# Kernel tuning notes

Hardware: AMD Instinct MI355X
Metric: run time of the kernel (lower is better)

The kernel has to match this reference:

```python
import jax, jax.numpy as jnp
import numpy as np

S, P, C, H, K = 16, 512, 768, 12, 6
D = C // H


def setup_inputs() -> dict:
    key = jax.random.key(0)
    k0, k1, k2 = jax.random.split(key, 3)
    x = jax.random.normal(k0, (1, S * P, C), jnp.float32)
    Wqkv = jax.random.normal(k1, (C, 3 * C), jnp.float32) * (C ** -0.5)
    bqkv = jnp.zeros((3 * C,), jnp.float32)
    Wproj = jax.random.normal(k2, (C, C), jnp.float32) * (C ** -0.5)
    bproj = jnp.zeros((C,), jnp.float32)
    # each frame i is covisible with K frames (itself + K-1 temporal neighbours)
    covis_idx = jnp.asarray((np.arange(S)[:, None] + np.arange(K)[None, :]) % S,
                            jnp.int32)  # [S, K]
    return {"x": x, "Wqkv": Wqkv, "bqkv": bqkv,
            "Wproj": Wproj, "bproj": bproj, "covis_idx": covis_idx}


def reference(x, Wqkv, bqkv, Wproj, bproj, covis_idx):
    B, N, C_ = x.shape
    S_, K_ = covis_idx.shape
    P_ = N // S_
    # qkv projection -> [3, B, H, N, D]
    qkv = (x @ Wqkv + bqkv).reshape(B, N, 3, H, D).transpose(2, 0, 3, 1, 4)
    q, k, v = qkv[0], qkv[1], qkv[2]
    kf = k.reshape(B, H, S_, P_, D)          # keys grouped by frame
    vf = v.reshape(B, H, S_, P_, D)
    qf = q.reshape(B, H, S_, P_, D).transpose(2, 0, 1, 3, 4)  # [S,B,H,P,D]
    scale = jnp.float32(D) ** -0.5

    def step(_, inp):
        q_i, idx = inp                        # q_i [B,H,P,D], idx [K]
        k_c = kf[:, :, idx].reshape(B, H, K_ * P_, D)   # gather covisible tokens
        v_c = vf[:, :, idx].reshape(B, H, K_ * P_, D)
        s = jnp.einsum('bhpd,bhnd->bhpn', q_i, k_c) * scale
        a = jax.nn.softmax(s, axis=-1)
        return None, jnp.einsum('bhpn,bhnd->bhpd', a, v_c)

    _, out = jax.lax.scan(step, None, (qf, covis_idx))  # [S,B,H,P,D]
    out = out.transpose(1, 0, 3, 2, 4).reshape(B, N, C_)  # [B, S*P, H*D]
    return out @ Wproj + bproj
```

## Files before the change

kernel.cpp:

```cpp
#include <hip/hip_runtime.h>
#include <stdint.h>

typedef __bf16 bf16;
typedef __bf16 bf16x4 __attribute__((ext_vector_type(4)));
typedef __bf16 bf16x8 __attribute__((ext_vector_type(8)));
typedef float floatx4 __attribute__((ext_vector_type(4)));
typedef short short4v __attribute__((ext_vector_type(4)));

#define NTOK 8192
#define HEADSZ 524288L

#if defined(__has_builtin)
#if __has_builtin(__builtin_amdgcn_mfma_f32_16x16x16bf16_1k)
#define HAVE_MFMA16_BUILTIN 1
#endif
#endif
__device__ __forceinline__ floatx4 mfma16(short4v a, short4v b, floatx4 c) {
#ifdef HAVE_MFMA16_BUILTIN
  return __builtin_amdgcn_mfma_f32_16x16x16bf16_1k(a, b, c, 0, 0, 0);
#else
  floatx4 d;
  asm("v_mfma_f32_16x16x16_bf16 %0, %1, %2, %3" : "=v"(d) : "v"(a), "v"(b), "v"(c));
  return d;
#endif
}

__device__ __forceinline__ void gload16(const bf16* g, bf16* l) {
  __builtin_amdgcn_global_load_lds(
      (const __attribute__((address_space(1))) uint8_t*)g,
      (__attribute__((address_space(3))) uint8_t*)l, 16, 0, 0);
}

__global__ void detect_kernel(const unsigned short* __restrict__ x, int* __restrict__ flag) {
  int lane = threadIdx.x & 63;
  int cnt = 0;
#pragma unroll
  for (int i = 0; i < 4; ++i) {
    unsigned int u = x[2 * (lane * 4 + i)];
    float v = __uint_as_float(u << 16);
    if (!(fabsf(v) <= 1e4f)) cnt++;
  }
#pragma unroll
  for (int off = 1; off < 64; off <<= 1) cnt += __shfl_xor(cnt, off, 64);
  if (threadIdx.x == 0) *flag = (cnt > 32) ? 1 : 0;
}

__global__ __launch_bounds__(256) void ingest_kernel(
    const void* s0, const void* s1, const void* s2, const void* s3, const void* s4,
    bf16* d0, bf16* d1, bf16* d2, bf16* d3, bf16* d4,
    const int* __restrict__ flag) {
  const long b0 = 6291456, b1 = b0 + 1769472, b2 = b1 + 2304, b3 = b2 + 589824, b4 = b3 + 768;
  long g = ((long)blockIdx.x * 256 + threadIdx.x) * 8;
  if (g >= b4) return;
  const void* src; bf16* dst; long off;
  if (g < b0)      { src = s0; dst = d0; off = g; }
  else if (g < b1) { src = s1; dst = d1; off = g - b0; }
  else if (g < b2) { src = s2; dst = d2; off = g - b1; }
  else if (g < b3) { src = s3; dst = d3; off = g - b2; }
  else             { src = s4; dst = d4; off = g - b3; }
  if (*flag) {
    const float* s = (const float*)src + off;
#pragma unroll
    for (int e = 0; e < 8; ++e) dst[off + e] = (bf16)s[e];
  } else {
    *(uint4*)(dst + off) = *(const uint4*)((const bf16*)src + off);
  }
}

__global__ __launch_bounds__(256) void transpose_kernel(
    const bf16* __restrict__ in, bf16* __restrict__ out, int R, int Ccols) {
  __shared__ bf16 t[32][33];
  int bx = blockIdx.x * 32, by = blockIdx.y * 32;
  int tx = threadIdx.x & 31, ty = threadIdx.x >> 5;
#pragma unroll
  for (int i = ty; i < 32; i += 8) t[i][tx] = in[(long)(by + i) * Ccols + bx + tx];
  __syncthreads();
#pragma unroll
  for (int i = ty; i < 32; i += 8) out[(long)(bx + i) * R + by + tx] = t[tx][i];
}

template <int EPI>
__global__ __launch_bounds__(256, 2) void gemm_kernel(
    const bf16* __restrict__ A, const bf16* __restrict__ BT,
    const bf16* __restrict__ bias, void* __restrict__ Cout,
    int M, int N, int Kd, const int* __restrict__ flag) {
  __shared__ bf16 As[128 * 32];
  __shared__ bf16 Bs[128 * 32];
  const int tid = threadIdx.x;
  const int w = tid >> 6, lane = tid & 63;
  const int quad = lane >> 4, l15 = lane & 15;
  const int m0 = blockIdx.x * 128, n0 = blockIdx.y * 128;
  const int wm = w >> 1, wn = w & 1;
  const int srow = lane >> 2;
  const int scol = (lane & 3) * 8;

  floatx4 acc[4][4] = {};
  const bf16* ga = A + (long)(m0 + 32 * w + srow) * Kd + scol;
  const bf16* gb = BT + (long)(n0 + 32 * w + srow) * Kd + scol;
  bf16* la = As + 32 * w * 32;
  bf16* lb = Bs + 32 * w * 32;

  for (int kk = 0; kk < Kd; kk += 32) {
    __syncthreads();
    gload16(ga + kk, la);
    gload16(ga + kk + 16 * Kd, la + 16 * 32);
    gload16(gb + kk, lb);
    gload16(gb + kk + 16 * Kd, lb + 16 * 32);
    __syncthreads();
    bf16x8 fa[4], fb[4];
#pragma unroll
    for (int i = 0; i < 4; ++i)
      fa[i] = *(const bf16x8*)(As + (64 * wm + 16 * i + l15) * 32 + quad * 8);
#pragma unroll
    for (int j = 0; j < 4; ++j)
      fb[j] = *(const bf16x8*)(Bs + (64 * wn + 16 * j + l15) * 32 + quad * 8);
#pragma unroll
    for (int i = 0; i < 4; ++i)
#pragma unroll
      for (int j = 0; j < 4; ++j)
        acc[i][j] = __builtin_amdgcn_mfma_f32_16x16x32_bf16(fa[i], fb[j], acc[i][j], 0, 0, 0);
  }

  const bool outf32 = (EPI == 0) && (flag[0] != 0);
#pragma unroll
  for (int i = 0; i < 4; ++i) {
#pragma unroll
    for (int j = 0; j < 4; ++j) {
      const int col = n0 + 64 * wn + 16 * j + l15;
      const float bv = (float)bias[col];
#pragma unroll
      for (int r = 0; r < 4; ++r) {
        const int row = m0 + 64 * wm + 16 * i + quad * 4 + r;
        const float v = acc[i][j][r] + bv;
        if (EPI == 1) {
          const int which = col / 768;
          const int rem = col - which * 768;
          const int hh = rem >> 6, d = rem & 63;
          const long base = ((long)which * 12 + hh) * HEADSZ + (long)(row >> 6) * 4096;
          long off;
          if (which < 2)
            off = base + (d >> 3) * 512 + (row & 63) * 8 + (d & 7);
          else
            off = base + ((row & 63) >> 3) * 512 + d * 8 + (row & 7);
          ((bf16*)Cout)[off] = (bf16)v;
        } else {
          if (outf32) ((float*)Cout)[(long)row * N + col] = v;
          else        ((bf16*)Cout)[(long)row * N + col] = (bf16)v;
        }
      }
    }
  }
}

__global__ __launch_bounds__(256, 2) void attn_kernel(
    const bf16* __restrict__ qkv, const int* __restrict__ covis,
    bf16* __restrict__ attnout) {
  __shared__ bf16 Ks[8192];
  __shared__ bf16 Vs[8192];

  const int tid = threadIdx.x;
  const int w = tid >> 6, lane = tid & 63;
  const int quad = lane >> 4, l15 = lane & 15;
  const int sb = w >> 1, hf = w & 1;

  const int xcd = blockIdx.x & 7;
  const int idx = blockIdx.x >> 3;
  const int qt = idx & 7;
  const int fh = xcd * 24 + (idx >> 3);
  const int h = fh >> 4, f = fh & 15;
  const int qtb = f * 8 + qt;

  const bf16* qb = qkv + (long)(0 * 12 + h) * HEADSZ;
  const bf16* kb = qkv + (long)(1 * 12 + h) * HEADSZ;
  const bf16* vb = qkv + (long)(2 * 12 + h) * HEADSZ;

  int frames[6];
#pragma unroll
  for (int j = 0; j < 6; ++j) frames[j] = covis[f * 6 + j];

  bf16x8 qa[2][4];
  {
    const bf16* qblk = qb + (long)qtb * 4096;
#pragma unroll
    for (int s = 0; s < 2; ++s)
#pragma unroll
      for (int nt = 0; nt < 4; ++nt)
        qa[s][nt] = *(const bf16x8*)(qblk + (4 * s + quad) * 512 + (nt * 16 + l15) * 8);
  }

  floatx4 o[16] = {};
  float rsum[4] = {0.f, 0.f, 0.f, 0.f};

  const int krow = 32 * hf + l15;
  for (int c = 0; c < 24; ++c) {
    const int tb0 = frames[c >> 2] * 8 + (c & 3) * 2;
    __syncthreads();
    {
      const bf16* kg = kb + (long)tb0 * 4096 + w * 2048;
      const bf16* vg = vb + (long)tb0 * 4096 + w * 2048;
#pragma unroll
      for (int i = 0; i < 4; ++i) gload16(kg + i * 512 + lane * 8, Ks + w * 2048 + i * 512);
#pragma unroll
      for (int i = 0; i < 4; ++i) gload16(vg + i * 512 + lane * 8, Vs + w * 2048 + i * 512);
    }
    __syncthreads();

#pragma unroll
    for (int mt = 0; mt < 2; ++mt) {
      floatx4 st[4] = {};
#pragma unroll
      for (int s = 0; s < 2; ++s) {
        bf16x8 kf = *(const bf16x8*)(Ks + ((sb * 8 + 4 * s + quad) * 64 + krow + 16 * mt) * 8);
#pragma unroll
        for (int nt = 0; nt < 4; ++nt)
          st[nt] = __builtin_amdgcn_mfma_f32_16x16x32_bf16(kf, qa[s][nt], st[nt], 0, 0, 0);
      }
      short4v p[4];
#pragma unroll
      for (int nt = 0; nt < 4; ++nt) {
        bf16x4 pb;
#pragma unroll
        for (int r = 0; r < 4; ++r) {
          float e = __builtin_amdgcn_exp2f(st[nt][r] * 0.18033688011112042f);
          pb[r] = (bf16)e;
          rsum[nt] += e;
        }
        p[nt] = __builtin_bit_cast(short4v, pb);
      }
#pragma unroll
      for (int mtd = 0; mtd < 4; ++mtd) {
        bf16x4 vf = *(const bf16x4*)(Vs + ((sb * 8 + 4 * hf + 2 * mt + (quad >> 1)) * 64 +
                                           mtd * 16 + l15) * 8 + (quad & 1) * 4);
        short4v va = __builtin_bit_cast(short4v, vf);
#pragma unroll
        for (int nt = 0; nt < 4; ++nt)
          o[mtd * 4 + nt] = mfma16(va, p[nt], o[mtd * 4 + nt]);
      }
    }
  }

  __syncthreads();
  float* sc = (float*)Ks;
#pragma unroll
  for (int nt = 0; nt < 4; ++nt) {
    rsum[nt] += __shfl_xor(rsum[nt], 16, 64);
    rsum[nt] += __shfl_xor(rsum[nt], 32, 64);
    sc[(w * 4 + nt) * 64 + lane] = rsum[nt];
  }
  __syncthreads();
  float inv[4];
#pragma unroll
  for (int nt = 0; nt < 4; ++nt) {
    float tot = sc[nt * 64 + lane] + sc[(4 + nt) * 64 + lane] +
                sc[(8 + nt) * 64 + lane] + sc[(12 + nt) * 64 + lane];
    inv[nt] = 1.0f / tot;
  }
  __syncthreads();

  float* buf0 = (float*)Ks;
  float* buf1 = (float*)Vs;
  if (w == 2) {
#pragma unroll
    for (int t = 0; t < 16; ++t) *(floatx4*)(buf0 + (t * 64 + lane) * 4) = o[t];
  } else if (w == 3) {
#pragma unroll
    for (int t = 0; t < 16; ++t) *(floatx4*)(buf1 + (t * 64 + lane) * 4) = o[t];
  }
  __syncthreads();
  if (w == 0) {
#pragma unroll
    for (int t = 0; t < 16; ++t) o[t] += *(const floatx4*)(buf0 + (t * 64 + lane) * 4);
  } else if (w == 1) {
#pragma unroll
    for (int t = 0; t < 16; ++t) o[t] += *(const floatx4*)(buf1 + (t * 64 + lane) * 4);
  }
  __syncthreads();
  if (w == 1) {
#pragma unroll
    for (int t = 0; t < 16; ++t) *(floatx4*)(buf0 + (t * 64 + lane) * 4) = o[t];
  }
  __syncthreads();
  if (w == 0) {
    bf16* ob = (bf16*)Vs;
#pragma unroll
    for (int mtd = 0; mtd < 4; ++mtd)
#pragma unroll
      for (int nt = 0; nt < 4; ++nt) {
        floatx4 t = o[mtd * 4 + nt] + *(const floatx4*)(buf0 + ((mtd * 4 + nt) * 64 + lane) * 4);
        bf16x4 bv;
#pragma unroll
        for (int r = 0; r < 4; ++r) bv[r] = (bf16)(t[r] * inv[nt]);
        *(bf16x4*)(ob + (nt * 16 + l15) * 64 + mtd * 16 + quad * 4) = bv;
      }
    bf16* dst = attnout + ((long)qtb * 64 + lane) * 768 + h * 64;
#pragma unroll
    for (int i = 0; i < 8; ++i)
      *(bf16x8*)(dst + i * 8) = *(const bf16x8*)(ob + lane * 64 + i * 8);
  }
}

extern "C" void kernel_launch(void* const* d_in, const int* in_sizes, int n_in,
                              void* d_out, int out_size, void* d_ws, size_t ws_size,
                              hipStream_t stream) {
  const void* x     = d_in[0];
  const void* Wqkv  = d_in[1];
  const void* bqkv  = d_in[2];
  const void* Wproj = d_in[3];
  const void* bproj = d_in[4];
  const int*  covis = (const int*)d_in[5];

  char* ws = (char*)d_ws;
  size_t off = 0;
  auto alloc = [&](size_t bytes) {
    char* p = ws + off;
    off += (bytes + 255) & ~(size_t)255;
    return p;
  };
  int*  flag   = (int*)alloc(256);
  bf16* xc     = (bf16*)alloc(6291456UL * 2);
  bf16* Wqkvc  = (bf16*)alloc(1769472UL * 2);
  bf16* bqkvc  = (bf16*)alloc(2304UL * 2);
  bf16* Wprojc = (bf16*)alloc(589824UL * 2);
  bf16* bprojc = (bf16*)alloc(768UL * 2);
  bf16* WqkvT  = (bf16*)alloc(1769472UL * 2);
  bf16* WprojT = (bf16*)alloc(589824UL * 2);
  bf16* qkvws  = (bf16*)alloc(3UL * 12 * 8192 * 64 * 2);
  bf16* attnw  = (bf16*)alloc(6291456UL * 2);

  detect_kernel<<<1, 64, 0, stream>>>((const unsigned short*)x, flag);
  ingest_kernel<<<4226, 256, 0, stream>>>(x, Wqkv, bqkv, Wproj, bproj,
                                          xc, Wqkvc, bqkvc, Wprojc, bprojc, flag);
  transpose_kernel<<<dim3(72, 24), 256, 0, stream>>>(Wqkvc, WqkvT, 768, 2304);
  transpose_kernel<<<dim3(24, 24), 256, 0, stream>>>(Wprojc, WprojT, 768, 768);
  gemm_kernel<1><<<dim3(64, 18), 256, 0, stream>>>(xc, WqkvT, bqkvc, qkvws, 8192, 2304, 768, flag);
  attn_kernel<<<1536, 256, 0, stream>>>(qkvws, covis, attnw);
  gemm_kernel<0><<<dim3(64, 6), 256, 0, stream>>>(attnw, WprojT, bprojc, d_out, 8192, 768, 768, flag);
}
```

Measured before the change: 283.4 us.

## Double-buffer attention K/V loads, fold scale into Q, fuse weight conversion

The attention kernel now double-buffers K/V tiles in shared memory so the next chunk's async loads are issued before computing the current one, and one of the two barriers per iteration is removed. The softmax scale is folded into the Q projection epilogue, and row sums are computed with an MFMA against a ones vector instead of scalar adds and shuffles. Weight fp32-to-bf16 conversion is merged into the transpose kernels, which drops an intermediate copy pass. Shared memory per block doubles, which may reduce occupancy. The single remaining barrier sits before the next issue, and the wait for async loads to land may be relying on that same barrier being placed correctly.

```diff
diff --git a/kernel.cpp b/kernel.cpp
--- a/kernel.cpp
+++ b/kernel.cpp
@@ -46,18 +46,15 @@
 }
 
 __global__ __launch_bounds__(256) void ingest_kernel(
-    const void* s0, const void* s1, const void* s2, const void* s3, const void* s4,
-    bf16* d0, bf16* d1, bf16* d2, bf16* d3, bf16* d4,
-    const int* __restrict__ flag) {
-  const long b0 = 6291456, b1 = b0 + 1769472, b2 = b1 + 2304, b3 = b2 + 589824, b4 = b3 + 768;
+    const void* s0, const void* s1, const void* s2,
+    bf16* d0, bf16* d1, bf16* d2, const int* __restrict__ flag) {
+  const long b0 = 6291456, b1 = b0 + 2304, b2 = b1 + 768;
   long g = ((long)blockIdx.x * 256 + threadIdx.x) * 8;
-  if (g >= b4) return;
+  if (g >= b2) return;
   const void* src; bf16* dst; long off;
   if (g < b0)      { src = s0; dst = d0; off = g; }
   else if (g < b1) { src = s1; dst = d1; off = g - b0; }
-  else if (g < b2) { src = s2; dst = d2; off = g - b1; }
-  else if (g < b3) { src = s3; dst = d3; off = g - b2; }
-  else             { src = s4; dst = d4; off = g - b3; }
+  else             { src = s2; dst = d2; off = g - b1; }
   if (*flag) {
     const float* s = (const float*)src + off;
 #pragma unroll
@@ -67,13 +64,18 @@
   }
 }
 
-__global__ __launch_bounds__(256) void transpose_kernel(
-    const bf16* __restrict__ in, bf16* __restrict__ out, int R, int Ccols) {
+__global__ __launch_bounds__(256) void transposeW_kernel(
+    const void* __restrict__ in, bf16* __restrict__ out, int R, int Ccols,
+    const int* __restrict__ flag) {
   __shared__ bf16 t[32][33];
   int bx = blockIdx.x * 32, by = blockIdx.y * 32;
   int tx = threadIdx.x & 31, ty = threadIdx.x >> 5;
-#pragma unroll
-  for (int i = ty; i < 32; i += 8) t[i][tx] = in[(long)(by + i) * Ccols + bx + tx];
+  const bool f32 = (*flag != 0);
+#pragma unroll
+  for (int i = ty; i < 32; i += 8) {
+    long src = (long)(by + i) * Ccols + bx + tx;
+    t[i][tx] = f32 ? (bf16)((const float*)in)[src] : ((const bf16*)in)[src];
+  }
   __syncthreads();
 #pragma unroll
   for (int i = ty; i < 32; i += 8) out[(long)(bx + i) * R + by + tx] = t[tx][i];
@@ -131,9 +133,10 @@
 #pragma unroll
       for (int r = 0; r < 4; ++r) {
         const int row = m0 + 64 * wm + 16 * i + quad * 4 + r;
-        const float v = acc[i][j][r] + bv;
+        float v = acc[i][j][r] + bv;
         if (EPI == 1) {
           const int which = col / 768;
+          if (which == 0) v *= 0.18033688011112042f;
           const int rem = col - which * 768;
           const int hh = rem >> 6, d = rem & 63;
           const long base = ((long)which * 12 + hh) * HEADSZ + (long)(row >> 6) * 4096;
@@ -155,8 +158,7 @@
 __global__ __launch_bounds__(256, 2) void attn_kernel(
     const bf16* __restrict__ qkv, const int* __restrict__ covis,
     bf16* __restrict__ attnout) {
-  __shared__ bf16 Ks[8192];
-  __shared__ bf16 Vs[8192];
+  __shared__ bf16 db[2][16384];
 
   const int tid = threadIdx.x;
   const int w = tid >> 6, lane = tid & 63;
@@ -188,22 +190,33 @@
         qa[s][nt] = *(const bf16x8*)(qblk + (4 * s + quad) * 512 + (nt * 16 + l15) * 8);
   }
 
+  bf16x4 ones4;
+#pragma unroll
+  for (int e = 0; e < 4; ++e) ones4[e] = (bf16)1.0f;
+  const short4v onesv = __builtin_bit_cast(short4v, ones4);
+
   floatx4 o[16] = {};
-  float rsum[4] = {0.f, 0.f, 0.f, 0.f};
+  floatx4 osum[4] = {};
 
   const int krow = 32 * hf + l15;
+
+  auto issue = [&](int c) {
+    const int tb0 = frames[c >> 2] * 8 + (c & 3) * 2;
+    bf16* base = db[c & 1];
+    const bf16* kg = kb + (long)tb0 * 4096 + w * 2048;
+    const bf16* vg = vb + (long)tb0 * 4096 + w * 2048;
+#pragma unroll
+    for (int i = 0; i < 4; ++i) gload16(kg + i * 512 + lane * 8, base + w * 2048 + i * 512);
+#pragma unroll
+    for (int i = 0; i < 4; ++i) gload16(vg + i * 512 + lane * 8, base + 8192 + w * 2048 + i * 512);
+  };
+
+  issue(0);
   for (int c = 0; c < 24; ++c) {
-    const int tb0 = frames[c >> 2] * 8 + (c & 3) * 2;
     __syncthreads();
-    {
-      const bf16* kg = kb + (long)tb0 * 4096 + w * 2048;
-      const bf16* vg = vb + (long)tb0 * 4096 + w * 2048;
-#pragma unroll
-      for (int i = 0; i < 4; ++i) gload16(kg + i * 512 + lane * 8, Ks + w * 2048 + i * 512);
-#pragma unroll
-      for (int i = 0; i < 4; ++i) gload16(vg + i * 512 + lane * 8, Vs + w * 2048 + i * 512);
-    }
-    __syncthreads();
+    if (c < 23) issue(c + 1);
+    const bf16* Ks = db[c & 1];
+    const bf16* Vs = db[c & 1] + 8192;
 
 #pragma unroll
     for (int mt = 0; mt < 2; ++mt) {
@@ -220,13 +233,11 @@
       for (int nt = 0; nt < 4; ++nt) {
         bf16x4 pb;
 #pragma unroll
-        for (int r = 0; r < 4; ++r) {
-          float e = __builtin_amdgcn_exp2f(st[nt][r] * 0.18033688011112042f);
-          pb[r] = (bf16)e;
-          rsum[nt] += e;
-        }
+        for (int r = 0; r < 4; ++r) pb[r] = (bf16)__builtin_amdgcn_exp2f(st[nt][r]);
         p[nt] = __builtin_bit_cast(short4v, pb);
       }
+#pragma unroll
+      for (int nt = 0; nt < 4; ++nt) osum[nt] = mfma16(onesv, p[nt], osum[nt]);
 #pragma unroll
       for (int mtd = 0; mtd < 4; ++mtd) {
         bf16x4 vf = *(const bf16x4*)(Vs + ((sb * 8 + 4 * hf + 2 * mt + (quad >> 1)) * 64 +
@@ -240,13 +251,9 @@
   }
 
   __syncthreads();
-  float* sc = (float*)Ks;
-#pragma unroll
-  for (int nt = 0; nt < 4; ++nt) {
-    rsum[nt] += __shfl_xor(rsum[nt], 16, 64);
-    rsum[nt] += __shfl_xor(rsum[nt], 32, 64);
-    sc[(w * 4 + nt) * 64 + lane] = rsum[nt];
-  }
+  float* sc = (float*)db[1];
+#pragma unroll
+  for (int nt = 0; nt < 4; ++nt) sc[(w * 4 + nt) * 64 + lane] = osum[nt][0];
   __syncthreads();
   float inv[4];
 #pragma unroll
@@ -257,8 +264,8 @@
   }
   __syncthreads();
 
-  float* buf0 = (float*)Ks;
-  float* buf1 = (float*)Vs;
+  float* buf0 = (float*)db[0];
+  float* buf1 = (float*)(db[0] + 8192);
   if (w == 2) {
 #pragma unroll
     for (int t = 0; t < 16; ++t) *(floatx4*)(buf0 + (t * 64 + lane) * 4) = o[t];
@@ -281,7 +288,7 @@
   }
   __syncthreads();
   if (w == 0) {
-    bf16* ob = (bf16*)Vs;
+    bf16* ob = (bf16*)db[1];
 #pragma unroll
     for (int mtd = 0; mtd < 4; ++mtd)
 #pragma unroll
@@ -318,9 +325,7 @@
   };
   int*  flag   = (int*)alloc(256);
   bf16* xc     = (bf16*)alloc(6291456UL * 2);
-  bf16* Wqkvc  = (bf16*)alloc(1769472UL * 2);
   bf16* bqkvc  = (bf16*)alloc(2304UL * 2);
-  bf16* Wprojc = (bf16*)alloc(589824UL * 2);
   bf16* bprojc = (bf16*)alloc(768UL * 2);
   bf16* WqkvT  = (bf16*)alloc(1769472UL * 2);
   bf16* WprojT = (bf16*)alloc(589824UL * 2);
@@ -328,10 +333,9 @@
   bf16* attnw  = (bf16*)alloc(6291456UL * 2);
 
   detect_kernel<<<1, 64, 0, stream>>>((const unsigned short*)x, flag);
-  ingest_kernel<<<4226, 256, 0, stream>>>(x, Wqkv, bqkv, Wproj, bproj,
-                                          xc, Wqkvc, bqkvc, Wprojc, bprojc, flag);
-  transpose_kernel<<<dim3(72, 24), 256, 0, stream>>>(Wqkvc, WqkvT, 768, 2304);
-  transpose_kernel<<<dim3(24, 24), 256, 0, stream>>>(Wprojc, WprojT, 768, 768);
+  ingest_kernel<<<3074, 256, 0, stream>>>(x, bqkv, bproj, xc, bqkvc, bprojc, flag);
+  transposeW_kernel<<<dim3(72, 24), 256, 0, stream>>>(Wqkv, WqkvT, 768, 2304, flag);
+  transposeW_kernel<<<dim3(24, 24), 256, 0, stream>>>(Wproj, WprojT, 768, 768, flag);
   gemm_kernel<1><<<dim3(64, 18), 256, 0, stream>>>(xc, WqkvT, bqkvc, qkvws, 8192, 2304, 768, flag);
   attn_kernel<<<1536, 256, 0, stream>>>(qkvws, covis, attnw);
   gemm_kernel<0><<<dim3(64, 6), 256, 0, stream>>>(attnw, WprojT, bprojc, d_out, 8192, 768, 768, flag);
```

After: 278.0 us. No clear change (-1.9%).
